# Kernel optimization log

Measured on AMD Instinct MI355X. Metric: run time of the kernel, lower is better.

## Reference

```python
import math
import jax, jax.numpy as jnp
import numpy as np

B, N_PER, FEAT, EMB, HEADS, E = 64, 512, 128, 128, 3, 131072
NEG = -1e9


def _gat(x, src, dst, emask, W, a_src, a_dst, bias):
    # PyG GATConv (concat heads, add_self_loops=True, negative_slope=0.2, eval mode -> no dropout)
    n = x.shape[0]
    H, C = a_src.shape
    h = (x @ W).reshape(n, H, C)                      # [n,H,C]
    e_src = (h * a_src[None]).sum(-1)                 # [n,H]
    e_dst = (h * a_dst[None]).sum(-1)                 # [n,H]
    loop = jnp.arange(n)
    s = jnp.concatenate([src, loop])
    d = jnp.concatenate([dst, loop])
    m = jnp.concatenate([emask, jnp.ones((n,), dtype=bool)])
    logit = jax.nn.leaky_relu(e_src[s] + e_dst[d], negative_slope=0.2)  # [E+n,H]
    logit = jnp.where(m[:, None], logit, NEG)
    mx = jax.ops.segment_max(logit, d, num_segments=n)
    ex = jnp.exp(logit - mx[d]) * m[:, None].astype(logit.dtype)
    den = jax.ops.segment_sum(ex, d, num_segments=n)
    alpha = ex / (den[d] + 1e-16)                     # edge-softmax over incoming edges
    out = jax.ops.segment_sum(alpha[:, :, None] * h[s], d, num_segments=n)
    return out.reshape(n, H * C) + bias


def _topk_pool(x, src, dst, emask, ratio, w):
    # PyG TopKPooling: score = tanh(x.w/||w||), keep ceil(ratio*n) per graph, gate kept x by score
    n = x.shape[0]
    per = n // B
    score = jnp.tanh((x @ w) / jnp.linalg.norm(w))    # [n]
    k = int(math.ceil(ratio * per))
    _, idx = jax.lax.top_k(score.reshape(B, per), k)  # [B,k]
    perm = (idx + (jnp.arange(B) * per)[:, None]).reshape(-1)
    xn = x[perm] * score[perm][:, None]
    newid = jnp.full((n,), -1, dtype=jnp.int32).at[perm].set(jnp.arange(B * k, dtype=jnp.int32))
    ns, nd = newid[src], newid[dst]
    valid = emask & (ns >= 0) & (nd >= 0)
    src = jnp.where(valid, ns, 0)
    dst = jnp.where(valid, nd, 0)
    batch = jnp.repeat(jnp.arange(B, dtype=jnp.int32), k)
    return xn, src, dst, valid, batch


def _gpool(x, batch):
    # cat([global_max_pool, global_mean_pool])
    mx = jax.ops.segment_max(x, batch, num_segments=B)
    sm = jax.ops.segment_sum(x, batch, num_segments=B)
    cnt = jax.ops.segment_sum(jnp.ones((x.shape[0], 1), x.dtype), batch, num_segments=B)
    return jnp.concatenate([mx, sm / cnt], axis=1)


def _forward(x, edge_attr, edge_index, batch_index, params):
    (W1, as1, ad1, b1, Wh1, bh1, pw1,
     W2, as2, ad2, b2, Wh2, bh2, pw2,
     W3, as3, ad3, b3, Wh3, bh3, pw3,
     Wl1, bl1, Wl2, bl2) = params
    src, dst = edge_index[0], edge_index[1]
    emask = jnp.ones((src.shape[0],), dtype=bool)

    h = _gat(x, src, dst, emask, W1, as1, ad1, b1)
    h = jax.nn.relu(h @ Wh1 + bh1)
    h, src, dst, emask, batch = _topk_pool(h, src, dst, emask, 0.8, pw1)
    x1 = _gpool(h, batch)

    h = _gat(h, src, dst, emask, W2, as2, ad2, b2)
    h = jax.nn.relu(h @ Wh2 + bh2)
    h, src, dst, emask, batch = _topk_pool(h, src, dst, emask, 0.5, pw2)
    x2 = _gpool(h, batch)

    h = _gat(h, src, dst, emask, W3, as3, ad3, b3)
    h = jax.nn.relu(h @ Wh3 + bh3)
    h, src, dst, emask, batch = _topk_pool(h, src, dst, emask, 0.2, pw3)
    x3 = _gpool(h, batch)

    z = x1 + x2 + x3
    z = jax.nn.relu(z @ Wl1 + bl1)
    # F.dropout p=0.8 skipped (eval mode)
    return z @ Wl2 + bl2


def setup_inputs() -> dict:
    key = jax.random.key(0)
    ks = jax.random.split(key, 32)
    e_per = E // B
    e = jax.random.randint(ks[0], (2, B, e_per), 0, N_PER) + (jnp.arange(B) * N_PER)[None, :, None]
    edge_index = e.reshape(2, E).astype(jnp.int32)
    inp = {
        'x': jax.random.normal(ks[1], (B * N_PER, FEAT), dtype=jnp.float32),
        'edge_attr': jnp.zeros((E, 1), dtype=jnp.float32),
        'edge_index': edge_index,
        'batch_index': jnp.repeat(jnp.arange(B, dtype=jnp.int32), N_PER),
    }
    def rn(k, shape, s=0.1):
        return jax.random.normal(k, shape, dtype=jnp.float32) * s
    names = ['W1','as1','ad1','b1','Wh1','bh1','pw1',
             'W2','as2','ad2','b2','Wh2','bh2','pw2',
             'W3','as3','ad3','b3','Wh3','bh3','pw3',
             'Wl1','bl1','Wl2','bl2']
    shapes = [(FEAT, HEADS*EMB), (HEADS, EMB), (HEADS, EMB), (HEADS*EMB,), (HEADS*EMB, EMB), (EMB,), (EMB,),
              (EMB, HEADS*EMB), (HEADS, EMB), (HEADS, EMB), (HEADS*EMB,), (HEADS*EMB, EMB), (EMB,), (EMB,),
              (EMB, HEADS*EMB), (HEADS, EMB), (HEADS, EMB), (HEADS*EMB,), (HEADS*EMB, EMB), (EMB,), (EMB,),
              (2*EMB, 512), (512,), (512, 256), (256,)]
    for i, (nm, sh) in enumerate(zip(names, shapes)):
        inp[nm] = rn(ks[2 + i], sh)
    return inp


def reference(x, edge_attr, edge_index, batch_index,
              W1, as1, ad1, b1, Wh1, bh1, pw1,
              W2, as2, ad2, b2, Wh2, bh2, pw2,
              W3, as3, ad3, b3, Wh3, bh3, pw3,
              Wl1, bl1, Wl2, bl2):
    params = (W1, as1, ad1, b1, Wh1, bh1, pw1,
              W2, as2, ad2, b2, Wh2, bh2, pw2,
              W3, as3, ad3, b3, Wh3, bh3, pw3,
              Wl1, bl1, Wl2, bl2)
    return _forward(x, edge_attr, edge_index, batch_index, params)
```

## Files before the change

### kernel.cpp

```cpp
#include <hip/hip_runtime.h>
#include <cfloat>

static __device__ __forceinline__ float lrelu(float v) { return v >= 0.f ? v : 0.2f * v; }

typedef __attribute__((ext_vector_type(8))) short bf16x8;
typedef __attribute__((ext_vector_type(8))) unsigned short ushort8;
typedef __attribute__((ext_vector_type(4))) float f32x4;

__device__ __forceinline__ unsigned short f2bf(float x) {
    unsigned u = __float_as_uint(x);
    u += 0x7FFF + ((u >> 16) & 1);
    return (unsigned short)(u >> 16);
}
__device__ __forceinline__ float bf2f(unsigned short h) {
    return __uint_as_float(((unsigned)h) << 16);
}

struct SegT { const float* s; unsigned short* dh; unsigned short* dl; int rows, cols, tr; };
struct Segs { SegT seg[7]; int cum[8]; };

__global__ __launch_bounds__(256) void split_k(Segs S, int total)
{
    int idx = blockIdx.x * 256 + threadIdx.x;
    if (idx >= total) return;
    int si = 0;
    while (idx >= S.cum[si + 1]) si++;
    int o = idx - S.cum[si];
    SegT g = S.seg[si];
    float v = g.s[o];
    unsigned short h = f2bf(v);
    unsigned short l = f2bf(v - bf2f(h));
    int di = o;
    if (g.tr) { int r = o / g.cols, c = o - r * g.cols; di = c * g.rows + r; }
    g.dh[di] = h;
    g.dl[di] = l;
}

struct WaArgs { const float* W[3]; const float* as_[3]; const float* ad_[3]; const float* pw[3]; };

__global__ __launch_bounds__(256) void wa_k(WaArgs a, float* __restrict__ wab, float* __restrict__ rn)
{
    int wid = blockIdx.x * 4 + (threadIdx.x >> 6);
    int lane = threadIdx.x & 63;
    if (wid < 2304) {
        int l = wid / 768, r = wid - l * 768;
        int j = r >> 7, kk = r & 127;
        int hh = j % 3;
        const float* av = (j < 3 ? a.as_[l] : a.ad_[l]) + hh * 128;
        const float* Wp = a.W[l] + (size_t)kk * 384 + hh * 128;
        float p = Wp[lane] * av[lane] + Wp[lane + 64] * av[lane + 64];
#pragma unroll
        for (int o = 32; o > 0; o >>= 1) p += __shfl_down(p, o);
        if (lane == 0) wab[l * 768 + j * 128 + kk] = p;
    } else if (wid < 2307) {
        int l = wid - 2304;
        const float* pw = a.pw[l];
        float v0 = pw[lane], v1 = pw[lane + 64];
        float p = v0 * v0 + v1 * v1;
#pragma unroll
        for (int o = 32; o > 0; o >>= 1) p += __shfl_down(p, o);
        if (lane == 0) rn[l] = 1.f / sqrtf(p);
    }
}

__global__ __launch_bounds__(256) void esd_k(const float* __restrict__ X,
                                             const float* __restrict__ wab,
                                             float* __restrict__ es, float* __restrict__ ed, int n)
{
    int wid = (int)((blockIdx.x * 256 + threadIdx.x) >> 6);
    int lane = threadIdx.x & 63;
    if (wid >= n) return;
    const float* xp = X + (size_t)wid * 128;
    float x0 = xp[lane], x1 = xp[lane + 64];
    float p[6];
#pragma unroll
    for (int j = 0; j < 6; j++)
        p[j] = x0 * wab[j * 128 + lane] + x1 * wab[j * 128 + 64 + lane];
#pragma unroll
    for (int o = 32; o > 0; o >>= 1)
#pragma unroll
        for (int j = 0; j < 6; j++) p[j] += __shfl_down(p[j], o);
    if (lane == 0) {
#pragma unroll
        for (int h = 0; h < 3; h++) { es[(size_t)wid * 3 + h] = p[h]; ed[(size_t)wid * 3 + h] = p[h + 3]; }
    }
}

__global__ __launch_bounds__(256) void gemm_bf2_k(const unsigned short* __restrict__ AH,
                                                  const unsigned short* __restrict__ AL,
                                                  const unsigned short* __restrict__ BTH,
                                                  const unsigned short* __restrict__ BTL,
                                                  const float* __restrict__ bias,
                                                  float* __restrict__ C,
                                                  int M, int K, int N, int relu,
                                                  const float* __restrict__ pwv,
                                                  const float* __restrict__ rnormp,
                                                  float* __restrict__ scv)
{
    __shared__ unsigned short sAH[64 * 32], sAL[64 * 32];
    __shared__ unsigned short sBH[128 * 32], sBL[128 * 32];
    __shared__ float sred[2][64];
    const int tid  = threadIdx.x;
    const int lane = tid & 63;
    const int wave = tid >> 6;
    const int wr = (wave >> 1) * 32;
    const int wc = (wave & 1) * 64;
    const int row0 = blockIdx.x * 64, col0 = blockIdx.y * 128;

    f32x4 acc[2][4];
#pragma unroll
    for (int i = 0; i < 2; i++)
#pragma unroll
        for (int j = 0; j < 4; j++) acc[i][j] = (f32x4){0.f, 0.f, 0.f, 0.f};

    const int a_r = tid >> 2;
    const int a_c = tid & 3;
    const int a_slot = a_r * 32 + ((a_c ^ ((a_r ^ (a_r >> 2)) & 3)) << 3);
    const unsigned short* ApH = AH + (size_t)(row0 + a_r) * K + a_c * 8;
    const unsigned short* ApL = AL + (size_t)(row0 + a_r) * K + a_c * 8;

    const int b_c = tid >> 1;
    const int b_h = (tid & 1) * 2;
    const int b_sw = (b_c ^ (b_c >> 2)) & 3;
    const unsigned short* BpH = BTH + (size_t)(col0 + b_c) * K + b_h * 8;
    const unsigned short* BpL = BTL + (size_t)(col0 + b_c) * K + b_h * 8;

    const int l15 = lane & 15;
    const int kc  = lane >> 4;

    for (int k0 = 0; k0 < K; k0 += 32) {
        ushort8 vah = *reinterpret_cast<const ushort8*>(ApH + k0);
        ushort8 val = *reinterpret_cast<const ushort8*>(ApL + k0);
        ushort8 vb[4];
        vb[0] = *reinterpret_cast<const ushort8*>(BpH + k0);
        vb[1] = *reinterpret_cast<const ushort8*>(BpH + k0 + 8);
        vb[2] = *reinterpret_cast<const ushort8*>(BpL + k0);
        vb[3] = *reinterpret_cast<const ushort8*>(BpL + k0 + 8);

        __syncthreads();

        *reinterpret_cast<ushort8*>(&sAH[a_slot]) = vah;
        *reinterpret_cast<ushort8*>(&sAL[a_slot]) = val;
        {
            int s0 = b_c * 32 + (((b_h + 0) ^ b_sw) << 3);
            int s1 = b_c * 32 + (((b_h + 1) ^ b_sw) << 3);
            *reinterpret_cast<ushort8*>(&sBH[s0]) = vb[0];
            *reinterpret_cast<ushort8*>(&sBH[s1]) = vb[1];
            *reinterpret_cast<ushort8*>(&sBL[s0]) = vb[2];
            *reinterpret_cast<ushort8*>(&sBL[s1]) = vb[3];
        }
        __syncthreads();

        bf16x8 aH[2], aL[2], bH[4], bL[4];
#pragma unroll
        for (int fi = 0; fi < 2; fi++) {
            int r = wr + fi * 16 + l15;
            int sidx = r * 32 + ((kc ^ ((r ^ (r >> 2)) & 3)) << 3);
            aH[fi] = *reinterpret_cast<const bf16x8*>(&sAH[sidx]);
            aL[fi] = *reinterpret_cast<const bf16x8*>(&sAL[sidx]);
        }
#pragma unroll
        for (int fj = 0; fj < 4; fj++) {
            int c = wc + fj * 16 + l15;
            int sidx = c * 32 + ((kc ^ ((c ^ (c >> 2)) & 3)) << 3);
            bH[fj] = *reinterpret_cast<const bf16x8*>(&sBH[sidx]);
            bL[fj] = *reinterpret_cast<const bf16x8*>(&sBL[sidx]);
        }
#pragma unroll
        for (int fi = 0; fi < 2; fi++)
#pragma unroll
            for (int fj = 0; fj < 4; fj++) {
                acc[fi][fj] = __builtin_amdgcn_mfma_f32_16x16x32_bf16(aH[fi], bH[fj], acc[fi][fj], 0, 0, 0);
                acc[fi][fj] = __builtin_amdgcn_mfma_f32_16x16x32_bf16(aH[fi], bL[fj], acc[fi][fj], 0, 0, 0);
                acc[fi][fj] = __builtin_amdgcn_mfma_f32_16x16x32_bf16(aL[fi], bH[fj], acc[fi][fj], 0, 0, 0);
            }
    }

    float pwl[4];
    if (scv) {
#pragma unroll
        for (int fj = 0; fj < 4; fj++) pwl[fj] = pwv[wc + fj * 16 + l15];
    }
    float pd[2][4] = {{0.f,0.f,0.f,0.f},{0.f,0.f,0.f,0.f}};
#pragma unroll
    for (int fi = 0; fi < 2; fi++) {
        int rbase = row0 + wr + fi * 16 + (lane >> 4) * 4;
#pragma unroll
        for (int q = 0; q < 4; q++) {
            int r = rbase + q;
#pragma unroll
            for (int fj = 0; fj < 4; fj++) {
                int c = col0 + wc + fj * 16 + l15;
                float v = acc[fi][fj][q];
                if (bias) v += bias[c];
                if (relu) v = fmaxf(v, 0.f);
                C[(size_t)r * N + c] = v;
                if (scv) pd[fi][q] += v * pwl[fj];
            }
        }
    }
    if (scv) {
        float rn0 = rnormp[0];
#pragma unroll
        for (int fi = 0; fi < 2; fi++)
#pragma unroll
            for (int q = 0; q < 4; q++) {
                float s = pd[fi][q];
                s += __shfl_xor(s, 1);
                s += __shfl_xor(s, 2);
                s += __shfl_xor(s, 4);
                s += __shfl_xor(s, 8);
                if (l15 == 0) sred[wc >> 6][wr + fi * 16 + (lane >> 4) * 4 + q] = s;
            }
        __syncthreads();
        if (tid < 64)
            scv[row0 + tid] = tanhf((sred[0][tid] + sred[1][tid]) * rn0);
    }
}

__global__ __launch_bounds__(256) void gemm_small_k(const float* __restrict__ A,
                                                    const float* __restrict__ B,
                                                    const float* __restrict__ bias,
                                                    float* __restrict__ C,
                                                    int M, int K, int N, int relu)
{
    int idx = blockIdx.x * 256 + threadIdx.x;
    if (idx >= M * N) return;
    int r = idx / N, c = idx - r * N;
    const float* ap = A + (size_t)r * K;
    const float* bp = B + c;
    float s = 0.f;
#pragma unroll 8
    for (int k = 0; k < K; k++) s += ap[k] * bp[(size_t)k * N];
    if (bias) s += bias[c];
    if (relu) s = fmaxf(s, 0.f);
    C[idx] = s;
}

__global__ __launch_bounds__(256) void csr_k(const int* __restrict__ src,
                                             const int* __restrict__ dst,
                                             const int* __restrict__ valid,
                                             const float* __restrict__ es,
                                             const float* __restrict__ ed,
                                             int* __restrict__ csr,
                                             int* __restrict__ beg,
                                             int* __restrict__ end,
                                             float* __restrict__ wmx,
                                             float* __restrict__ winv,
                                             float* __restrict__ wself,
                                             int per)
{
    __shared__ int sdeg[512];
    __shared__ int soff[512];
    __shared__ float ses[1536];
    __shared__ float sed[1536];
    const int g = blockIdx.x;
    const int t = threadIdx.x;
    const int bn = g * per;
    const int be = g * 2048;
    for (int i = t; i < 512; i += 256) sdeg[i] = 0;
    for (int i = t; i < per * 3; i += 256) {
        ses[i] = es[(size_t)bn * 3 + i];
        sed[i] = ed[(size_t)bn * 3 + i];
    }
    __syncthreads();
#pragma unroll
    for (int j = 0; j < 8; j++) {
        int e = be + j * 256 + t;
        if (!valid || valid[e]) atomicAdd(&sdeg[dst[e] - bn], 1);
    }
    __syncthreads();
    const int i0 = t, i1 = t + 256;
    soff[i0] = sdeg[i0]; soff[i1] = sdeg[i1];
    __syncthreads();
    for (int d = 1; d < 512; d <<= 1) {
        int a0 = (i0 >= d) ? soff[i0 - d] : 0;
        int a1 = (i1 >= d) ? soff[i1 - d] : 0;
        __syncthreads();
        soff[i0] += a0; soff[i1] += a1;
        __syncthreads();
    }
    int excl0 = 0, excl1 = 0;
    if (i0 < per) { int dg = sdeg[i0]; excl0 = soff[i0] - dg; beg[bn + i0] = be + excl0; end[bn + i0] = be + excl0 + dg; }
    if (i1 < per) { int dg = sdeg[i1]; excl1 = soff[i1] - dg; beg[bn + i1] = be + excl1; end[bn + i1] = be + excl1 + dg; }
    __syncthreads();
    if (i0 < per) { soff[i0] = excl0; sdeg[i0] = excl0; }
    if (i1 < per) { soff[i1] = excl1; sdeg[i1] = excl1; }
    __syncthreads();
#pragma unroll
    for (int j = 0; j < 8; j++) {
        int e = be + j * 256 + t;
        if (!valid || valid[e]) {
            int p = atomicAdd(&sdeg[dst[e] - bn], 1);
            csr[be + p] = e;
        }
    }
    __syncthreads();
    for (int i = t; i < per; i += 256) {
        float edv[3], m[3], den[3], selfl[3];
#pragma unroll
        for (int h = 0; h < 3; h++) {
            edv[h] = sed[i * 3 + h];
            selfl[h] = lrelu(ses[i * 3 + h] + edv[h]);
            m[h] = selfl[h];
            den[h] = 1.f;
        }
        const int pb = soff[i], pe = sdeg[i];
        for (int p = pb; p < pe; p++) {
            int e = csr[be + p];
            int sl = src[e] - bn;
#pragma unroll
            for (int h = 0; h < 3; h++) {
                float l = lrelu(ses[sl * 3 + h] + edv[h]);
                if (l <= m[h]) den[h] += __expf(l - m[h]);
                else { den[h] = den[h] * __expf(m[h] - l) + 1.f; m[h] = l; }
            }
        }
#pragma unroll
        for (int h = 0; h < 3; h++) {
            float inv = 1.f / (den[h] + 1e-16f);
            wmx[(size_t)(bn + i) * 3 + h] = m[h];
            winv[(size_t)(bn + i) * 3 + h] = inv;
            wself[(size_t)(bn + i) * 3 + h] = __expf(selfl[h] - m[h]) * inv;
        }
    }
}

__global__ __launch_bounds__(256) void agg2_k(const float* __restrict__ H,
                                              const float* __restrict__ es,
                                              const float* __restrict__ ed,
                                              const float* __restrict__ wmx,
                                              const float* __restrict__ winv,
                                              const float* __restrict__ wself,
                                              const int* __restrict__ beg,
                                              const int* __restrict__ end,
                                              const int* __restrict__ csr,
                                              const int* __restrict__ srcArr,
                                              const float* __restrict__ bias,
                                              unsigned short* __restrict__ outH,
                                              unsigned short* __restrict__ outL, int n)
{
    int nwg = gridDim.x;
    int bid = blockIdx.x;
    int swz = (bid & 7) * (nwg >> 3) + (bid >> 3);
    int wid = swz * 4 + (int)(threadIdx.x >> 6);
    int lane = threadIdx.x & 63;
    if (wid >= n) return;
    const int d = wid;
    float edv[3], mxv[3], ivv[3], wsf[3];
#pragma unroll
    for (int h = 0; h < 3; h++) {
        edv[h] = ed[(size_t)d * 3 + h];
        mxv[h] = wmx[(size_t)d * 3 + h];
        ivv[h] = winv[(size_t)d * 3 + h];
        wsf[h] = wself[(size_t)d * 3 + h];
    }
    float acc[6];
    const float* hp = H + (size_t)d * 384;
#pragma unroll
    for (int j = 0; j < 6; j++) acc[j] = wsf[j >> 1] * hp[lane + 64 * j];
    const int pb = beg[d], pe = end[d];
    for (int p = pb; p < pe; p++) {
        int eg = csr[p];
        int s = srcArr[eg];
        float w[3];
#pragma unroll
        for (int h = 0; h < 3; h++) {
            float l = lrelu(es[(size_t)s * 3 + h] + edv[h]);
            w[h] = __expf(l - mxv[h]) * ivv[h];
        }
        const float* sp = H + (size_t)s * 384;
        acc[0] += w[0] * sp[lane];
        acc[1] += w[0] * sp[lane + 64];
        acc[2] += w[1] * sp[lane + 128];
        acc[3] += w[1] * sp[lane + 192];
        acc[4] += w[2] * sp[lane + 256];
        acc[5] += w[2] * sp[lane + 320];
    }
#pragma unroll
    for (int j = 0; j < 6; j++) {
        float v = acc[j] + bias[lane + 64 * j];
        unsigned short h = f2bf(v);
        outH[(size_t)d * 384 + lane + 64 * j] = h;
        outL[(size_t)d * 384 + lane + 64 * j] = f2bf(v - bf2f(h));
    }
}

__global__ __launch_bounds__(512) void select_k(const float* __restrict__ sc,
                                                const int* __restrict__ s_old,
                                                const int* __restrict__ d_old,
                                                const int* __restrict__ v_old,
                                                int per, int k,
                                                int* __restrict__ perm, float* __restrict__ ps,
                                                int* __restrict__ s_new,
                                                int* __restrict__ d_new,
                                                int* __restrict__ v_new)
{
    __shared__ float ss[512];
    __shared__ int sid[512];
    __shared__ int snew[512];
    const int b = blockIdx.x;
    const int t = threadIdx.x;
    const int bn = b * per;

    ss[t] = (t < per) ? sc[bn + t] : -FLT_MAX;
    sid[t] = (t < per) ? t : 512 + t;
    __syncthreads();
    for (int kk = 2; kk <= 512; kk <<= 1)
        for (int j = kk >> 1; j > 0; j >>= 1) {
            int ixj = t ^ j;
            if (ixj > t) {
                float a = ss[t], bq = ss[ixj];
                int ia = sid[t], ib = sid[ixj];
                bool aBefore = (a > bq) || (a == bq && ia < ib);
                bool up = ((t & kk) == 0);
                if (up ? !aBefore : aBefore) { ss[t] = bq; ss[ixj] = a; sid[t] = ib; sid[ixj] = ia; }
            }
            __syncthreads();
        }
    if (sid[t] < per) snew[sid[t]] = (t < k) ? (b * k + t) : -1;
    if (t < k) {
        perm[b * k + t] = bn + sid[t];
        ps[b * k + t] = ss[t];
    }
    __syncthreads();

    if (s_new) {
        const int be = b * 2048;
#pragma unroll
        for (int j = 0; j < 4; j++) {
            int e = be + j * 512 + t;
            int v = v_old ? v_old[e] : 1;
            int ns = -1, nd = -1;
            if (v) { ns = snew[s_old[e] - bn]; nd = snew[d_old[e] - bn]; }
            int ok = (v && ns >= 0 && nd >= 0) ? 1 : 0;
            s_new[e] = ok ? ns : 0;
            d_new[e] = ok ? nd : 0;
            v_new[e] = ok;
        }
    }
}

__global__ __launch_bounds__(256) void gate_k(const float* __restrict__ H,
                                              const int* __restrict__ perm,
                                              const float* __restrict__ ps,
                                              float* __restrict__ X,
                                              unsigned short* __restrict__ XH,
                                              unsigned short* __restrict__ XL, int nNew)
{
    int wid = (int)((blockIdx.x * 256 + threadIdx.x) >> 6);
    int lane = threadIdx.x & 63;
    if (wid >= nNew) return;
    int o = perm[wid];
    float g = ps[wid];
    float v0 = H[(size_t)o * 128 + lane] * g;
    float v1 = H[(size_t)o * 128 + 64 + lane] * g;
    X[(size_t)wid * 128 + lane] = v0;
    X[(size_t)wid * 128 + 64 + lane] = v1;
    unsigned short h0 = f2bf(v0), h1 = f2bf(v1);
    XH[(size_t)wid * 128 + lane] = h0;
    XH[(size_t)wid * 128 + 64 + lane] = h1;
    XL[(size_t)wid * 128 + lane] = f2bf(v0 - bf2f(h0));
    XL[(size_t)wid * 128 + 64 + lane] = f2bf(v1 - bf2f(h1));
}

__global__ __launch_bounds__(1024) void gpool_k(const float* __restrict__ X,
                                                float* __restrict__ z, int k, int first)
{
    __shared__ float smx[8][128];
    __shared__ float ssm[8][128];
    const int b = blockIdx.x;
    const int col = threadIdx.x & 127;
    const int rg = threadIdx.x >> 7;
    const float* xp = X + (size_t)b * k * 128 + col;
    float mx = -FLT_MAX, sm = 0.f;
    int r = rg;
#pragma unroll 4
    for (; r + 32 <= k; r += 32) {
        float v0 = xp[(size_t)(r + 0)  * 128];
        float v1 = xp[(size_t)(r + 8)  * 128];
        float v2 = xp[(size_t)(r + 16) * 128];
        float v3 = xp[(size_t)(r + 24) * 128];
        mx = fmaxf(fmaxf(fmaxf(mx, v0), fmaxf(v1, v2)), v3);
        sm += v0 + v1 + v2 + v3;
    }
    for (; r < k; r += 8) {
        float v = xp[(size_t)r * 128];
        mx = fmaxf(mx, v);
        sm += v;
    }
    smx[rg][col] = mx;
    ssm[rg][col] = sm;
    __syncthreads();
    if (rg == 0) {
#pragma unroll
        for (int i = 1; i < 8; i++) { mx = fmaxf(mx, smx[i][col]); sm += ssm[i][col]; }
        if (first) {
            z[b * 256 + col] = mx;
            z[b * 256 + 128 + col] = sm / (float)k;
        } else {
            z[b * 256 + col] += mx;
            z[b * 256 + 128 + col] += sm / (float)k;
        }
    }
}

extern "C" void kernel_launch(void* const* d_in, const int* in_sizes, int n_in,
                              void* d_out, int out_size, void* d_ws, size_t ws_size,
                              hipStream_t stream)
{
    (void)in_sizes; (void)n_in; (void)out_size; (void)ws_size;

    const float* x   = (const float*)d_in[0];
    const int*   ei  = (const int*)d_in[2];
    const float* W1  = (const float*)d_in[4];
    const float* as1 = (const float*)d_in[5];
    const float* ad1 = (const float*)d_in[6];
    const float* b1  = (const float*)d_in[7];
    const float* Wh1 = (const float*)d_in[8];
    const float* bh1 = (const float*)d_in[9];
    const float* pw1 = (const float*)d_in[10];
    const float* W2  = (const float*)d_in[11];
    const float* as2 = (const float*)d_in[12];
    const float* ad2 = (const float*)d_in[13];
    const float* b2  = (const float*)d_in[14];
    const float* Wh2 = (const float*)d_in[15];
    const float* bh2 = (const float*)d_in[16];
    const float* pw2 = (const float*)d_in[17];
    const float* W3  = (const float*)d_in[18];
    const float* as3 = (const float*)d_in[19];
    const float* ad3 = (const float*)d_in[20];
    const float* b3  = (const float*)d_in[21];
    const float* Wh3 = (const float*)d_in[22];
    const float* bh3 = (const float*)d_in[23];
    const float* pw3 = (const float*)d_in[24];
    const float* Wl1 = (const float*)d_in[25];
    const float* bl1 = (const float*)d_in[26];
    const float* Wl2 = (const float*)d_in[27];
    const float* bl2 = (const float*)d_in[28];
    float* out = (float*)d_out;

    const int E = 131072;
    const int n1 = 32768, per1 = 512, k1 = 410;
    const int n2 = 64 * k1, per2 = k1, k2 = 205;
    const int n3 = 64 * k2, per3 = k2, k3 = 41;
    const int n4 = 64 * k3;

    char* wsb = (char*)d_ws;
    size_t off = 0;
    auto alloc = [&](size_t bytes) -> void* {
        void* p = wsb + off;
        off += (bytes + 255) & ~(size_t)255;
        return p;
    };
    float* A    = (float*)alloc((size_t)n1 * 384 * 4);
    unsigned short* BfH = (unsigned short*)alloc((size_t)n1 * 384 * 2);
    unsigned short* BfL = (unsigned short*)alloc((size_t)n1 * 384 * 2);
    unsigned short* X0H = (unsigned short*)alloc((size_t)n1 * 128 * 2);
    unsigned short* X0L = (unsigned short*)alloc((size_t)n1 * 128 * 2);
    unsigned short* XaH = (unsigned short*)alloc((size_t)n2 * 128 * 2);
    unsigned short* XaL = (unsigned short*)alloc((size_t)n2 * 128 * 2);
    unsigned short* WT[6], *WTl[6];
    for (int i = 0; i < 6; i++) {
        WT[i]  = (unsigned short*)alloc((size_t)49152 * 2);
        WTl[i] = (unsigned short*)alloc((size_t)49152 * 2);
    }
    float* ES   = (float*)alloc((size_t)n1 * 3 * 4);
    float* ED   = (float*)alloc((size_t)n1 * 3 * 4);
    float* SC   = (float*)alloc((size_t)n1 * 4);
    int*   CSR  = (int*)alloc((size_t)E * 4);
    int*   BEG  = (int*)alloc((size_t)n1 * 4);
    int*   END  = (int*)alloc((size_t)n1 * 4);
    int*   SRCA = (int*)alloc((size_t)E * 4);
    int*   DSTA = (int*)alloc((size_t)E * 4);
    int*   VALA = (int*)alloc((size_t)E * 4);
    int*   SRCB = (int*)alloc((size_t)E * 4);
    int*   DSTB = (int*)alloc((size_t)E * 4);
    int*   VALB = (int*)alloc((size_t)E * 4);
    float* X1   = (float*)alloc((size_t)n2 * 128 * 4);
    float* X2   = (float*)alloc((size_t)n3 * 128 * 4);
    float* X3   = (float*)alloc((size_t)n4 * 128 * 4);
    int*   PERM = (int*)alloc((size_t)n2 * 4);
    float* PSC  = (float*)alloc((size_t)n2 * 4);
    float* WMX  = (float*)alloc((size_t)n1 * 3 * 4);
    float* WINV = (float*)alloc((size_t)n1 * 3 * 4);
    float* WSELF= (float*)alloc((size_t)n1 * 3 * 4);
    float* WAB  = (float*)alloc((size_t)2304 * 4);
    float* RN   = (float*)alloc((size_t)4 * 4);
    float* Z    = (float*)alloc((size_t)64 * 256 * 4);
    float* ZH   = (float*)alloc((size_t)64 * 512 * 4);

    {
        Segs S;
        const float* srcs[7] = {x, W1, Wh1, W2, Wh2, W3, Wh3};
        unsigned short* dh[7] = {X0H, WT[0], WT[1], WT[2], WT[3], WT[4], WT[5]};
        unsigned short* dl[7] = {X0L, WTl[0], WTl[1], WTl[2], WTl[3], WTl[4], WTl[5]};
        int rows[7] = {n1, 128, 384, 128, 384, 128, 384};
        int cols[7] = {128, 384, 128, 384, 128, 384, 128};
        int trs[7]  = {0, 1, 1, 1, 1, 1, 1};
        int cum = 0;
        for (int i = 0; i < 7; i++) {
            S.seg[i] = SegT{srcs[i], dh[i], dl[i], rows[i], cols[i], trs[i]};
            S.cum[i] = cum;
            cum += rows[i] * cols[i];
        }
        S.cum[7] = cum;
        split_k<<<(cum + 255) / 256, 256, 0, stream>>>(S, cum);

        WaArgs wa;
        wa.W[0] = W1;  wa.W[1] = W2;  wa.W[2] = W3;
        wa.as_[0] = as1; wa.as_[1] = as2; wa.as_[2] = as3;
        wa.ad_[0] = ad1; wa.ad_[1] = ad2; wa.ad_[2] = ad3;
        wa.pw[0] = pw1; wa.pw[1] = pw2; wa.pw[2] = pw3;
        wa_k<<<(2307 + 3) / 4, 256, 0, stream>>>(wa, WAB, RN);
    }

    auto layer = [&](const float* Xf, const unsigned short* xh, const unsigned short* xl,
                     int n, int per, int kk, int lidx,
                     const int* src, const int* dst, const int* val,
                     const unsigned short* wt, const unsigned short* wtl, const float* bb,
                     const unsigned short* wht, const unsigned short* whtl, const float* bh,
                     const float* pw,
                     float* Xn, unsigned short* XnH, unsigned short* XnL,
                     int* srcN, int* dstN, int* valN)
    {
        int nNew = 64 * kk;
        esd_k<<<n / 4, 256, 0, stream>>>(Xf, WAB + lidx * 768, ES, ED, n);
        gemm_bf2_k<<<dim3(n / 64, 3), 256, 0, stream>>>(xh, xl, wt, wtl, nullptr, A, n, 128, 384, 0,
                                                        nullptr, nullptr, nullptr);
        csr_k<<<64, 256, 0, stream>>>(src, dst, val, ES, ED, CSR, BEG, END, WMX, WINV, WSELF, per);
        agg2_k<<<n / 4, 256, 0, stream>>>(A, ES, ED, WMX, WINV, WSELF, BEG, END, CSR, src, bb, BfH, BfL, n);
        gemm_bf2_k<<<dim3(n / 64, 1), 256, 0, stream>>>(BfH, BfL, wht, whtl, bh, A, n, 384, 128, 1,
                                                        pw, RN + lidx, SC);
        select_k<<<64, 512, 0, stream>>>(SC, src, dst, val, per, kk, PERM, PSC, srcN, dstN, valN);
        gate_k<<<nNew / 4, 256, 0, stream>>>(A, PERM, PSC, Xn, XnH, XnL, nNew);
        gpool_k<<<64, 1024, 0, stream>>>(Xn, Z, kk, lidx == 0 ? 1 : 0);
    };

    layer(x,  X0H, X0L, n1, per1, k1, 0, ei,   ei + E, nullptr,
          WT[0], WTl[0], b1, WT[1], WTl[1], bh1, pw1,
          X1, XaH, XaL, SRCA, DSTA, VALA);
    layer(X1, XaH, XaL, n2, per2, k2, 1, SRCA, DSTA, VALA,
          WT[2], WTl[2], b2, WT[3], WTl[3], bh2, pw2,
          X2, XaH, XaL, SRCB, DSTB, VALB);
    layer(X2, XaH, XaL, n3, per3, k3, 2, SRCB, DSTB, VALB,
          WT[4], WTl[4], b3, WT[5], WTl[5], bh3, pw3,
          X3, XaH, XaL, nullptr, nullptr, nullptr);

    gemm_small_k<<<(64 * 512 + 255) / 256, 256, 0, stream>>>(Z,  Wl1, bl1, ZH,  64, 256, 512, 1);
    gemm_small_k<<<(64 * 256 + 255) / 256, 256, 0, stream>>>(ZH, Wl2, bl2, out, 64, 512, 256, 0);
}
```

Before: 391.1 us.

## Fuse attention logit dot-products into GEMM epilogue and merge pooling kernels

Removes the separate wa_k precompute and per-layer esd_k kernel. The per-head source and destination attention scores are now computed in the first GEMM's epilogue from the fp32 accumulators, reduced across lanes and through shared memory. The three per-layer global pooling launches are merged into one kernel at the end that reads X1, X2 and X3. This saves several launches and a re-read of the layer input, at the cost of extra epilogue work and an extra block barrier in the GEMM.

```diff
diff --git a/kernel.cpp b/kernel.cpp
--- a/kernel.cpp
+++ b/kernel.cpp
@@ -36,54 +36,18 @@
     g.dl[di] = l;
 }
 
-struct WaArgs { const float* W[3]; const float* as_[3]; const float* ad_[3]; const float* pw[3]; };
-
-__global__ __launch_bounds__(256) void wa_k(WaArgs a, float* __restrict__ wab, float* __restrict__ rn)
-{
-    int wid = blockIdx.x * 4 + (threadIdx.x >> 6);
-    int lane = threadIdx.x & 63;
-    if (wid < 2304) {
-        int l = wid / 768, r = wid - l * 768;
-        int j = r >> 7, kk = r & 127;
-        int hh = j % 3;
-        const float* av = (j < 3 ? a.as_[l] : a.ad_[l]) + hh * 128;
-        const float* Wp = a.W[l] + (size_t)kk * 384 + hh * 128;
-        float p = Wp[lane] * av[lane] + Wp[lane + 64] * av[lane + 64];
-#pragma unroll
-        for (int o = 32; o > 0; o >>= 1) p += __shfl_down(p, o);
-        if (lane == 0) wab[l * 768 + j * 128 + kk] = p;
-    } else if (wid < 2307) {
-        int l = wid - 2304;
-        const float* pw = a.pw[l];
-        float v0 = pw[lane], v1 = pw[lane + 64];
-        float p = v0 * v0 + v1 * v1;
-#pragma unroll
-        for (int o = 32; o > 0; o >>= 1) p += __shfl_down(p, o);
-        if (lane == 0) rn[l] = 1.f / sqrtf(p);
-    }
-}
-
-__global__ __launch_bounds__(256) void esd_k(const float* __restrict__ X,
-                                             const float* __restrict__ wab,
-                                             float* __restrict__ es, float* __restrict__ ed, int n)
-{
-    int wid = (int)((blockIdx.x * 256 + threadIdx.x) >> 6);
-    int lane = threadIdx.x & 63;
-    if (wid >= n) return;
-    const float* xp = X + (size_t)wid * 128;
-    float x0 = xp[lane], x1 = xp[lane + 64];
-    float p[6];
-#pragma unroll
-    for (int j = 0; j < 6; j++)
-        p[j] = x0 * wab[j * 128 + lane] + x1 * wab[j * 128 + 64 + lane];
-#pragma unroll
-    for (int o = 32; o > 0; o >>= 1)
-#pragma unroll
-        for (int j = 0; j < 6; j++) p[j] += __shfl_down(p[j], o);
-    if (lane == 0) {
-#pragma unroll
-        for (int h = 0; h < 3; h++) { es[(size_t)wid * 3 + h] = p[h]; ed[(size_t)wid * 3 + h] = p[h + 3]; }
-    }
+__global__ __launch_bounds__(192) void rn3_k(const float* __restrict__ pw0,
+                                             const float* __restrict__ pw1,
+                                             const float* __restrict__ pw2,
+                                             float* __restrict__ rn)
+{
+    int l = threadIdx.x >> 6, lane = threadIdx.x & 63;
+    const float* pw = (l == 0) ? pw0 : ((l == 1) ? pw1 : pw2);
+    float v0 = pw[lane], v1 = pw[lane + 64];
+    float p = v0 * v0 + v1 * v1;
+#pragma unroll
+    for (int o = 32; o > 0; o >>= 1) p += __shfl_down(p, o);
+    if (lane == 0) rn[l] = 1.f / sqrtf(p);
 }
 
 __global__ __launch_bounds__(256) void gemm_bf2_k(const unsigned short* __restrict__ AH,
@@ -95,11 +59,15 @@
                                                   int M, int K, int N, int relu,
                                                   const float* __restrict__ pwv,
                                                   const float* __restrict__ rnormp,
-                                                  float* __restrict__ scv)
+                                                  float* __restrict__ scv,
+                                                  const float* __restrict__ asv,
+                                                  const float* __restrict__ adv,
+                                                  float* __restrict__ esv,
+                                                  float* __restrict__ edv)
 {
     __shared__ unsigned short sAH[64 * 32], sAL[64 * 32];
     __shared__ unsigned short sBH[128 * 32], sBL[128 * 32];
-    __shared__ float sred[2][64];
+    __shared__ float sred[4][64];
     const int tid  = threadIdx.x;
     const int lane = tid & 63;
     const int wave = tid >> 6;
@@ -176,12 +144,23 @@
             }
     }
 
-    float pwl[4];
+    float pwl[4], asl[4], adl[4];
     if (scv) {
 #pragma unroll
         for (int fj = 0; fj < 4; fj++) pwl[fj] = pwv[wc + fj * 16 + l15];
     }
-    float pd[2][4] = {{0.f,0.f,0.f,0.f},{0.f,0.f,0.f,0.f}};
+    const int hd = blockIdx.y;
+    if (esv) {
+#pragma unroll
+        for (int fj = 0; fj < 4; fj++) {
+            int cl = wc + fj * 16 + l15;
+            asl[fj] = asv[hd * 128 + cl];
+            adl[fj] = adv[hd * 128 + cl];
+        }
+    }
+    float pd[2][4]  = {{0.f,0.f,0.f,0.f},{0.f,0.f,0.f,0.f}};
+    float pds[2][4] = {{0.f,0.f,0.f,0.f},{0.f,0.f,0.f,0.f}};
+    float pdd[2][4] = {{0.f,0.f,0.f,0.f},{0.f,0.f,0.f,0.f}};
 #pragma unroll
     for (int fi = 0; fi < 2; fi++) {
         int rbase = row0 + wr + fi * 16 + (lane >> 4) * 4;
@@ -196,6 +175,7 @@
                 if (relu) v = fmaxf(v, 0.f);
                 C[(size_t)r * N + c] = v;
                 if (scv) pd[fi][q] += v * pwl[fj];
+                if (esv) { pds[fi][q] += v * asl[fj]; pdd[fi][q] += v * adl[fj]; }
             }
         }
     }
@@ -215,6 +195,34 @@
         __syncthreads();
         if (tid < 64)
             scv[row0 + tid] = tanhf((sred[0][tid] + sred[1][tid]) * rn0);
+    }
+    if (esv) {
+#pragma unroll
+        for (int fi = 0; fi < 2; fi++)
+#pragma unroll
+            for (int q = 0; q < 4; q++) {
+                float s = pds[fi][q];
+                s += __shfl_xor(s, 1);
+                s += __shfl_xor(s, 2);
+                s += __shfl_xor(s, 4);
+                s += __shfl_xor(s, 8);
+                float d = pdd[fi][q];
+                d += __shfl_xor(d, 1);
+                d += __shfl_xor(d, 2);
+                d += __shfl_xor(d, 4);
+                d += __shfl_xor(d, 8);
+                if (l15 == 0) {
+                    int rl = wr + fi * 16 + (lane >> 4) * 4 + q;
+                    sred[wc >> 6][rl] = s;
+                    sred[2 + (wc >> 6)][rl] = d;
+                }
+            }
+        __syncthreads();
+        if (tid < 64) {
+            int r = row0 + tid;
+            esv[(size_t)r * 3 + hd] = sred[0][tid] + sred[1][tid];
+            edv[(size_t)r * 3 + hd] = sred[2][tid] + sred[3][tid];
+        }
     }
 }
 
@@ -464,44 +472,54 @@
     XL[(size_t)wid * 128 + 64 + lane] = f2bf(v1 - bf2f(h1));
 }
 
-__global__ __launch_bounds__(1024) void gpool_k(const float* __restrict__ X,
-                                                float* __restrict__ z, int k, int first)
+__global__ __launch_bounds__(1024) void gpool3_k(const float* __restrict__ X1,
+                                                 const float* __restrict__ X2,
+                                                 const float* __restrict__ X3,
+                                                 int k1, int k2, int k3,
+                                                 float* __restrict__ z)
 {
     __shared__ float smx[8][128];
     __shared__ float ssm[8][128];
     const int b = blockIdx.x;
     const int col = threadIdx.x & 127;
     const int rg = threadIdx.x >> 7;
-    const float* xp = X + (size_t)b * k * 128 + col;
-    float mx = -FLT_MAX, sm = 0.f;
-    int r = rg;
+    const float* Xs[3] = {X1, X2, X3};
+    const int ks[3] = {k1, k2, k3};
+    float accm = 0.f, accs = 0.f;
+#pragma unroll
+    for (int L = 0; L < 3; L++) {
+        const int k = ks[L];
+        const float* xp = Xs[L] + (size_t)b * k * 128 + col;
+        float mx = -FLT_MAX, sm = 0.f;
+        int r = rg;
 #pragma unroll 4
-    for (; r + 32 <= k; r += 32) {
-        float v0 = xp[(size_t)(r + 0)  * 128];
-        float v1 = xp[(size_t)(r + 8)  * 128];
-        float v2 = xp[(size_t)(r + 16) * 128];
-        float v3 = xp[(size_t)(r + 24) * 128];
-        mx = fmaxf(fmaxf(fmaxf(mx, v0), fmaxf(v1, v2)), v3);
-        sm += v0 + v1 + v2 + v3;
-    }
-    for (; r < k; r += 8) {
-        float v = xp[(size_t)r * 128];
-        mx = fmaxf(mx, v);
-        sm += v;
-    }
-    smx[rg][col] = mx;
-    ssm[rg][col] = sm;
-    __syncthreads();
+        for (; r + 32 <= k; r += 32) {
+            float v0 = xp[(size_t)(r + 0)  * 128];
+            float v1 = xp[(size_t)(r + 8)  * 128];
+            float v2 = xp[(size_t)(r + 16) * 128];
+            float v3 = xp[(size_t)(r + 24) * 128];
+            mx = fmaxf(fmaxf(fmaxf(mx, v0), fmaxf(v1, v2)), v3);
+            sm += v0 + v1 + v2 + v3;
+        }
+        for (; r < k; r += 8) {
+            float v = xp[(size_t)r * 128];
+            mx = fmaxf(mx, v);
+            sm += v;
+        }
+        smx[rg][col] = mx;
+        ssm[rg][col] = sm;
+        __syncthreads();
+        if (rg == 0) {
+#pragma unroll
+            for (int i = 1; i < 8; i++) { mx = fmaxf(mx, smx[i][col]); sm += ssm[i][col]; }
+            accm += mx;
+            accs += sm / (float)k;
+        }
+        __syncthreads();
+    }
     if (rg == 0) {
-#pragma unroll
-        for (int i = 1; i < 8; i++) { mx = fmaxf(mx, smx[i][col]); sm += ssm[i][col]; }
-        if (first) {
-            z[b * 256 + col] = mx;
-            z[b * 256 + 128 + col] = sm / (float)k;
-        } else {
-            z[b * 256 + col] += mx;
-            z[b * 256 + 128 + col] += sm / (float)k;
-        }
+        z[b * 256 + col] = accm;
+        z[b * 256 + 128 + col] = accs;
     }
 }
 
@@ -585,7 +603,6 @@
     float* WMX  = (float*)alloc((size_t)n1 * 3 * 4);
     float* WINV = (float*)alloc((size_t)n1 * 3 * 4);
     float* WSELF= (float*)alloc((size_t)n1 * 3 * 4);
-    float* WAB  = (float*)alloc((size_t)2304 * 4);
     float* RN   = (float*)alloc((size_t)4 * 4);
     float* Z    = (float*)alloc((size_t)64 * 256 * 4);
     float* ZH   = (float*)alloc((size_t)64 * 512 * 4);
@@ -606,46 +623,43 @@
         }
         S.cum[7] = cum;
         split_k<<<(cum + 255) / 256, 256, 0, stream>>>(S, cum);
-
-        WaArgs wa;
-        wa.W[0] = W1;  wa.W[1] = W2;  wa.W[2] = W3;
-        wa.as_[0] = as1; wa.as_[1] = as2; wa.as_[2] = as3;
-        wa.ad_[0] = ad1; wa.ad_[1] = ad2; wa.ad_[2] = ad3;
-        wa.pw[0] = pw1; wa.pw[1] = pw2; wa.pw[2] = pw3;
-        wa_k<<<(2307 + 3) / 4, 256, 0, stream>>>(wa, WAB, RN);
-    }
-
-    auto layer = [&](const float* Xf, const unsigned short* xh, const unsigned short* xl,
+        rn3_k<<<1, 192, 0, stream>>>(pw1, pw2, pw3, RN);
+    }
+
+    auto layer = [&](const unsigned short* xh, const unsigned short* xl,
                      int n, int per, int kk, int lidx,
                      const int* src, const int* dst, const int* val,
-                     const unsigned short* wt, const unsigned short* wtl, const float* bb,
+                     const unsigned short* wt, const unsigned short* wtl,
+                     const float* as_, const float* ad_, const float* bb,
                      const unsigned short* wht, const unsigned short* whtl, const float* bh,
                      const float* pw,
                      float* Xn, unsigned short* XnH, unsigned short* XnL,
                      int* srcN, int* dstN, int* valN)
     {
         int nNew = 64 * kk;
-        esd_k<<<n / 4, 256, 0, stream>>>(Xf, WAB + lidx * 768, ES, ED, n);
         gemm_bf2_k<<<dim3(n / 64, 3), 256, 0, stream>>>(xh, xl, wt, wtl, nullptr, A, n, 128, 384, 0,
-                                                        nullptr, nullptr, nullptr);
+                                                        nullptr, nullptr, nullptr,
+                                                        as_, ad_, ES, ED);
         csr_k<<<64, 256, 0, stream>>>(src, dst, val, ES, ED, CSR, BEG, END, WMX, WINV, WSELF, per);
         agg2_k<<<n / 4, 256, 0, stream>>>(A, ES, ED, WMX, WINV, WSELF, BEG, END, CSR, src, bb, BfH, BfL, n);
         gemm_bf2_k<<<dim3(n / 64, 1), 256, 0, stream>>>(BfH, BfL, wht, whtl, bh, A, n, 384, 128, 1,
-                                                        pw, RN + lidx, SC);
+                                                        pw, RN + lidx, SC,
+                                                        nullptr, nullptr, nullptr, nullptr);
         select_k<<<64, 512, 0, stream>>>(SC, src, dst, val, per, kk, PERM, PSC, srcN, dstN, valN);
         gate_k<<<nNew / 4, 256, 0, stream>>>(A, PERM, PSC, Xn, XnH, XnL, nNew);
-        gpool_k<<<64, 1024, 0, stream>>>(Xn, Z, kk, lidx == 0 ? 1 : 0);
     };
 
-    layer(x,  X0H, X0L, n1, per1, k1, 0, ei,   ei + E, nullptr,
-          WT[0], WTl[0], b1, WT[1], WTl[1], bh1, pw1,
+    layer(X0H, X0L, n1, per1, k1, 0, ei,   ei + E, nullptr,
+          WT[0], WTl[0], as1, ad1, b1, WT[1], WTl[1], bh1, pw1,
           X1, XaH, XaL, SRCA, DSTA, VALA);
-    layer(X1, XaH, XaL, n2, per2, k2, 1, SRCA, DSTA, VALA,
-          WT[2], WTl[2], b2, WT[3], WTl[3], bh2, pw2,
+    layer(XaH, XaL, n2, per2, k2, 1, SRCA, DSTA, VALA,
+          WT[2], WTl[2], as2, ad2, b2, WT[3], WTl[3], bh2, pw2,
           X2, XaH, XaL, SRCB, DSTB, VALB);
-    layer(X2, XaH, XaL, n3, per3, k3, 2, SRCB, DSTB, VALB,
-          WT[4], WTl[4], b3, WT[5], WTl[5], bh3, pw3,
+    layer(XaH, XaL, n3, per3, k3, 2, SRCB, DSTB, VALB,
+          WT[4], WTl[4], as3, ad3, b3, WT[5], WTl[5], bh3, pw3,
           X3, XaH, XaL, nullptr, nullptr, nullptr);
+
+    gpool3_k<<<64, 1024, 0, stream>>>(X1, X2, X3, k1, k2, k3, Z);
 
     gemm_small_k<<<(64 * 512 + 255) / 256, 256, 0, stream>>>(Z,  Wl1, bl1, ZH,  64, 256, 512, 1);
     gemm_small_k<<<(64 * 256 + 255) / 256, 256, 0, stream>>>(ZH, Wl2, bl2, out, 64, 512, 256, 0);
```

Result: faster. 364.0 us (-6.9%).
